# Performance work log

Hardware: AMD Instinct MI355X
Metric: run time of the kernel (lower is better)

## Reference

```python
import jax, jax.numpy as jnp
import numpy as np

INV_SQRT2 = 0.7071067811865476  # 1/sqrt(2), haar filter coefficient
LEVEL = 2
EFF = 3          # effective modes per axis: (16 // omega=6) + 1
OUT_C = 64
SUBBANDS = ("aad", "ada", "add", "daa", "dad", "dda", "ddd")


def dwt1(x, axis):
    # Haar analysis along `axis` (even length, periodic => no padding needed).
    x = jnp.moveaxis(x, axis, -1)
    e, o = x[..., ::2], x[..., 1::2]
    a = (e + o) * INV_SQRT2
    d = (e - o) * INV_SQRT2
    return jnp.moveaxis(a, -1, axis), jnp.moveaxis(d, -1, axis)


def idwt1(a, d, axis):
    a = jnp.moveaxis(a, axis, -1)
    d = jnp.moveaxis(d, axis, -1)
    e = (a + d) * INV_SQRT2
    o = (a - d) * INV_SQRT2
    x = jnp.stack([e, o], axis=-1).reshape(e.shape[:-1] + (2 * e.shape[-1],))
    return jnp.moveaxis(x, -1, axis)


def dwt3(x):
    # One level of separable 3D DWT over last 3 axes -> dict of 8 subbands.
    ax, dx = dwt1(x, -3)
    out = {}
    for nx, tx in (("a", ax), ("d", dx)):
        ay, dy = dwt1(tx, -2)
        for ny, ty in (("a", ay), ("d", dy)):
            az, dz = dwt1(ty, -1)
            out[nx + ny + "a"] = az
            out[nx + ny + "d"] = dz
    return out


def idwt3(c):
    aa = idwt1(c["aaa"], c["aad"], -1)
    ad = idwt1(c["ada"], c["add"], -1)
    da = idwt1(c["daa"], c["dad"], -1)
    dd = idwt1(c["dda"], c["ddd"], -1)
    a = idwt1(aa, ad, -2)
    d = idwt1(da, dd, -2)
    return idwt1(a, d, -3)


def spectralconv(waves, w4):
    # waves: [B, Ci, X, Y, Z] real; w4: [4, Ci, Co, m, m, m] complex.
    B, Ci, X, Y, Z = waves.shape
    m = EFF
    xw = jnp.fft.rfftn(waves, axes=(-3, -2, -1))
    out = jnp.zeros((B, OUT_C, X, Y, Z // 2 + 1), dtype=xw.dtype)
    mul = lambda blk, w: jnp.einsum("bixyz,ioxyz->boxyz", blk, w)
    out = out.at[:, :, :m, :m, :m].set(mul(xw[:, :, :m, :m, :m], w4[0]))
    out = out.at[:, :, -m:, :m, :m].set(mul(xw[:, :, -m:, :m, :m], w4[1]))
    out = out.at[:, :, :m, -m:, :m].set(mul(xw[:, :, :m, -m:, :m], w4[2]))
    out = out.at[:, :, -m:, -m:, :m].set(mul(xw[:, :, -m:, -m:, :m], w4[3]))
    return jnp.fft.irfftn(out, s=(X, Y, Z), axes=(-3, -2, -1))


def _forward(x, weights):
    # weights: [8, 4, Ci, Co, m, m, m, 2] real -> complex [8, 4, Ci, Co, m, m, m]
    w = jax.lax.complex(weights[..., 0], weights[..., 1])
    # multi-level wavedec3: details[0] = finest, details[-1] = coarsest
    a = x
    details = []
    for _ in range(LEVEL):
        c = dwt3(a)
        a = c.pop("aaa")
        details.append(c)
    # spectral conv on coarsest approx + 7 coarsest detail subbands
    a = spectralconv(a, w[0])
    coarse = details[-1]
    details[-1] = {k: spectralconv(coarse[k], w[i + 1]) for i, k in enumerate(SUBBANDS)}
    # waverec3
    for c in reversed(details):
        full = dict(c)
        full["aaa"] = a
        a = idwt3(full)
    return a


def setup_inputs() -> dict:
    key = jax.random.key(0)
    kx, kw = jax.random.split(key)
    x = jax.random.normal(kx, (4, 64, 64, 64, 64), dtype=jnp.float32)
    scale = 1.0 / (64 * 64)
    weights = scale * jax.random.uniform(kw, (8, 4, 64, 64, 3, 3, 3, 2), dtype=jnp.float32)
    return {"x": x, "weights": weights}


def reference(x, weights):
    return _forward(x, weights)
```

## Files before the change

kernel.cpp:

```cpp
#include <hip/hip_runtime.h>


typedef float f32x4 __attribute__((ext_vector_type(4)));

__constant__ float C16c[16] = {
  1.0f, 0.92387953251128675f, 0.70710678118654752f, 0.38268343236508977f,
  0.0f, -0.38268343236508977f, -0.70710678118654752f, -0.92387953251128675f,
  -1.0f, -0.92387953251128675f, -0.70710678118654752f, -0.38268343236508977f,
  0.0f, 0.38268343236508977f, 0.70710678118654752f, 0.92387953251128675f
};
__constant__ float S16c[16] = {
  0.0f, 0.38268343236508977f, 0.70710678118654752f, 0.92387953251128675f,
  1.0f, 0.92387953251128675f, 0.70710678118654752f, 0.38268343236508977f,
  0.0f, -0.38268343236508977f, -0.70710678118654752f, -0.92387953251128675f,
  -1.0f, -0.92387953251128675f, -0.70710678118654752f, -0.38268343236508977f
};
__constant__ int KYv[6] = {0, 1, 2, 13, 14, 15};

__global__ __launch_bounds__(256) void k1_front(const float* __restrict__ x,
                                                float2* __restrict__ g2) {
  __shared__ float sm[8 * 16 * 17 + 8];
  __shared__ float2 fz[8 * 3 * 17];
  unsigned tid = threadIdx.x;
  unsigned px = blockIdx.x & 15u;
  unsigned bc = blockIdx.x >> 4;
  unsigned c = bc & 63u, b = bc >> 6;
  const f32x4* xp4 = (const f32x4*)(x + ((size_t)bc << 18)) + (size_t)px * 4096u;
  unsigned z4 = tid & 15u;
#pragma unroll
  for (int q = 0; q < 4; q++) {
    float a00 = 0.f, a01 = 0.f, a10 = 0.f, a11 = 0.f;
#pragma unroll
    for (int i = 0; i < 4; i++) {
      f32x4 v = xp4[i * 1024 + q * 256 + tid];
      float h0 = v.x + v.y, h1 = v.z + v.w;
      a00 += h0; a01 += h1;
      if (i < 2) { a10 += h0; a11 += h1; } else { a10 -= h0; a11 -= h1; }
    }
    float p00 = a00 + __shfl_xor(a00, 16);
    float p01 = a01 + __shfl_xor(a01, 16);
    float p10 = a10 + __shfl_xor(a10, 16);
    float p11 = a11 + __shfl_xor(a11, 16);
    float q00 = __shfl_xor(p00, 32), q01 = __shfl_xor(p01, 32);
    float q10 = __shfl_xor(p10, 32), q11 = __shfl_xor(p11, 32);
    bool hi = (tid >> 5) & 1u;
    float ya0 = p00 + q00, yd0 = hi ? (q00 - p00) : (p00 - q00);
    float ya1 = p01 + q01, yd1 = hi ? (q01 - p01) : (p01 - q01);
    float za0 = p10 + q10, zd0 = hi ? (q10 - p10) : (p10 - q10);
    float za1 = p11 + q11, zd1 = hi ? (q11 - p11) : (p11 - q11);
    if (((tid >> 4) & 3u) == 0u) {
      unsigned py = q * 4 + (tid >> 6);
      float* smp = sm + py * 17u + z4;
      smp[0 * 272] = (ya0 + ya1) * 0.125f;
      smp[1 * 272] = (ya0 - ya1) * 0.125f;
      smp[2 * 272] = (yd0 + yd1) * 0.125f;
      smp[3 * 272] = (yd0 - yd1) * 0.125f;
      smp[4 * 272] = (za0 + za1) * 0.125f;
      smp[5 * 272] = (za0 - za1) * 0.125f;
      smp[6 * 272] = (zd0 + zd1) * 0.125f;
      smp[7 * 272] = (zd0 - zd1) * 0.125f;
    }
  }
  __syncthreads();
  if (tid < 128u) {
    unsigned k = tid >> 4, y = tid & 15u;
    const float* row = sm + k * 272u + y * 17u;
#pragma unroll
    for (int kz = 0; kz < 3; kz++) {
      float re = 0.f, im = 0.f;
#pragma unroll
      for (int nz = 0; nz < 16; nz++) {
        float vv = row[nz];
        int t16 = (kz * nz) & 15;
        re += vv * C16c[t16];
        im -= vv * S16c[t16];
      }
      fz[k * 51u + kz * 17u + y] = make_float2(re, im);
    }
  }
  __syncthreads();
  if (tid < 144u) {
    unsigned k = tid / 18u, r = tid - k * 18u;
    unsigned kyi = r / 3u, kz = r - kyi * 3u;
    int ky = KYv[kyi];
    float re = 0.f, im = 0.f;
#pragma unroll
    for (int ny = 0; ny < 16; ny++) {
      float2 vv = fz[k * 51u + kz * 17u + ny];
      int t16 = (ky * ny) & 15;
      float cc = C16c[t16], sn = S16c[t16];
      re += vv.x * cc + vv.y * sn;
      im += vv.y * cc - vv.x * sn;
    }
    g2[(((size_t)b * 144u + tid) * 16u + px) * 64u + c] = make_float2(re, im);
  }
}

__global__ __launch_bounds__(256) void k2_mix(const float* __restrict__ w2,
                                              const float2* __restrict__ g2,
                                              float2* __restrict__ oh2) {
  __shared__ float2 ihl[4][64][27];
  unsigned tid = threadIdx.x;
  unsigned kc = blockIdx.x >> 3;
  unsigned ob = blockIdx.x & 7u;
  unsigned k = kc >> 2, corner = kc & 3u;
  unsigned kxi0 = 3u * (corner & 1u), kyi0 = 3u * (corner >> 1);
  {
    unsigned c = tid & 63u, b = tid >> 6;
    const float2* gb = g2 + ((size_t)b * 144u * 16u) * 64u + c;
#pragma unroll
    for (unsigned kyl = 0; kyl < 3u; kyl++) {
#pragma unroll
      for (unsigned kz = 0; kz < 3u; kz++) {
        unsigned row = k * 18u + (kyl + kyi0) * 3u + kz;
        float2 rg[16];
#pragma unroll
        for (int nx = 0; nx < 16; nx++) rg[nx] = gb[((size_t)row * 16u + nx) * 64u];
#pragma unroll
        for (unsigned kxl = 0; kxl < 3u; kxl++) {
          int kx = KYv[kxl + kxi0];
          float re = 0.f, im = 0.f;
#pragma unroll
          for (int nx = 0; nx < 16; nx++) {
            int t16 = (kx * nx) & 15;
            float cc = C16c[t16], sn = S16c[t16];
            re += rg[nx].x * cc + rg[nx].y * sn;
            im += rg[nx].y * cc - rg[nx].x * sn;
          }
          ihl[b][c][kxl * 9u + kyl * 3u + kz] = make_float2(re, im);
        }
      }
    }
  }
  __syncthreads();
  if (tid >= 216u) return;
  unsigned o = tid / 27u, f = tid - o * 27u;
  const float* wp = w2 + (((size_t)kc * 64u * 64u + (ob * 8u + o)) * 27u + f) * 2u;
  float2 acc[4];
#pragma unroll
  for (int b = 0; b < 4; b++) acc[b] = make_float2(0.f, 0.f);
#pragma unroll 8
  for (unsigned i = 0; i < 64u; i++) {
    float wr = __builtin_nontemporal_load(wp + (size_t)i * 3456u);
    float wi = __builtin_nontemporal_load(wp + (size_t)i * 3456u + 1u);
#pragma unroll
    for (int b = 0; b < 4; b++) {
      float2 a = ihl[b][i][f];
      acc[b].x += a.x * wr - a.y * wi;
      acc[b].y += a.x * wi + a.y * wr;
    }
  }
  unsigned kxl = f / 9u, kyl = (f - kxl * 9u) / 3u, kz = f % 3u;
  unsigned fg = (kxl + kxi0) * 18u + (kyl + kyi0) * 3u + kz;
#pragma unroll
  for (int b = 0; b < 4; b++)
    oh2[((size_t)(b * 64u + ob * 8u + o)) * 864u + k * 108u + fg] = acc[b];
}

__global__ __launch_bounds__(256) void k3_invsynth(const float2* __restrict__ oh2,
                                                   const float* __restrict__ x,
                                                   float* __restrict__ out) {
  __shared__ float2 hh[864];
  __shared__ float2 gx[2][8][18];
  __shared__ float2 uu[2][8][3][16];
  __shared__ float W[2][8][16][16];
  unsigned tid = threadIdx.x;
  unsigned sp = blockIdx.x & 7u;
  unsigned bo = 255u - (blockIdx.x >> 3);
  for (unsigned i = tid; i < 864u; i += 256u)
    hh[i] = oh2[(size_t)bo * 864u + i];
  __syncthreads();
  for (unsigned i = tid; i < 288u; i += 256u) {
    unsigned sl = i / 144u, j = i - sl * 144u;
    unsigned k = j / 18u, r = j - k * 18u;
    unsigned nx = sp * 2u + sl;
    float re = 0.f, im = 0.f;
#pragma unroll
    for (int kxi = 0; kxi < 6; kxi++) {
      float2 v = hh[k * 108u + kxi * 18 + r];
      int t16 = (KYv[kxi] * (int)nx) & 15;
      float cc = C16c[t16], sn = S16c[t16];
      re += v.x * cc - v.y * sn;
      im += v.x * sn + v.y * cc;
    }
    gx[sl][k][r] = make_float2(re, im);
  }
  __syncthreads();
  for (unsigned i = tid; i < 768u; i += 256u) {
    unsigned sl = i / 384u, j = i - sl * 384u;
    unsigned k = j / 48u, rem = j - k * 48u;
    unsigned kz = rem >> 4, ny = rem & 15u;
    float re = 0.f, im = 0.f;
#pragma unroll
    for (int kyi = 0; kyi < 6; kyi++) {
      float2 v = gx[sl][k][kyi * 3 + kz];
      int t16 = (KYv[kyi] * (int)ny) & 15;
      float cc = C16c[t16], sn = S16c[t16];
      re += v.x * cc - v.y * sn;
      im += v.x * sn + v.y * cc;
    }
    uu[sl][k][kz][ny] = make_float2(re, im);
  }
  __syncthreads();
  for (unsigned i = tid; i < 512u; i += 256u) {
    unsigned sl = i >> 8, ny = (i >> 4) & 15u, nz = i & 15u;
    float c1 = C16c[nz], s1 = S16c[nz];
    int t2 = (2 * nz) & 15;
    float c2 = C16c[t2], s2 = S16c[t2];
    float val[8];
#pragma unroll
    for (int k = 0; k < 8; k++) {
      float2 u0 = uu[sl][k][0][ny], u1 = uu[sl][k][1][ny], u2 = uu[sl][k][2][ny];
      val[k] = (u0.x + 2.f * (u1.x * c1 - u1.y * s1) + 2.f * (u2.x * c2 - u2.y * s2)) * (1.f / 4096.f);
    }
#pragma unroll
    for (int st = 1; st < 8; st <<= 1)
#pragma unroll
      for (int i2 = 0; i2 < 8; i2++)
        if (!(i2 & st)) {
          float a = val[i2], bb = val[i2 | st];
          val[i2] = a + bb;
          val[i2 | st] = a - bb;
        }
#pragma unroll
    for (int m = 0; m < 8; m++) W[sl][m][ny][nz] = val[m];
  }
  __syncthreads();
  unsigned w = tid >> 6, l = tid & 63u;
  unsigned z4 = l & 15u, y2 = l >> 4;
  unsigned mmy = ((y2 >> 1) & 1u) << 1;
  const float* xp = x + ((size_t)bo << 18);
  float* op = out + ((size_t)bo << 18);
#pragma unroll
  for (unsigned sl = 0; sl < 2u; ++sl) {
#pragma unroll
    for (unsigned r2 = 0; r2 < 8u; ++r2) {
      unsigned xp2 = r2 & 1u, yg = r2 >> 1;
      unsigned X0 = ((sp * 2u + sl) << 2) + (xp2 << 1);
      unsigned Y = (yg << 4) + (w << 2) + y2;
      size_t off = ((size_t)X0 << 12) + (Y << 6) + (z4 << 2);
      f32x4 v0 = *(const f32x4*)(xp + off);
      f32x4 v1 = *(const f32x4*)(xp + off + 4096u);
      float h0 = v0.x + v0.y + v1.x + v1.y;
      float h1 = v0.z + v0.w + v1.z + v1.w;
      float m0 = (h0 + __shfl_xor(h0, 16)) * 0.125f;
      float m1 = (h1 + __shfl_xor(h1, 16)) * 0.125f;
      unsigned ny = (yg << 2) + w;
      unsigned mm = (xp2 << 2) | mmy;
      float c0 = 0.125f * W[sl][mm][ny][z4] - m0;
      float c1 = 0.125f * W[sl][mm | 1u][ny][z4] - m1;
      v0.x += c0; v0.y += c0; v0.z += c1; v0.w += c1;
      v1.x += c0; v1.y += c0; v1.z += c1; v1.w += c1;
      __builtin_nontemporal_store(v0, (f32x4*)(op + off));
      __builtin_nontemporal_store(v1, (f32x4*)(op + off + 4096u));
    }
  }
}

extern "C" void kernel_launch(void* const* d_in, const int* in_sizes, int n_in,
                              void* d_out, int out_size, void* d_ws, size_t ws_size,
                              hipStream_t stream) {
  const float* x = (const float*)d_in[0];
  const float* w = (const float*)d_in[1];
  float* out = (float*)d_out;

  const size_t G_B = 4ull * 144 * 16 * 64 * 8;
  const size_t OH_B = 256ull * 864 * 8;

  float2 *g2, *oh2;
  char* ws = (char*)d_ws;
  if (ws_size >= G_B + OH_B) {
    g2 = (float2*)ws;
    oh2 = (float2*)(ws + G_B);
  } else {
    oh2 = (float2*)ws;
    g2 = (float2*)((char*)d_out + (size_t)out_size * 4 - G_B);
  }

  k1_front<<<4096, 256, 0, stream>>>(x, g2);
  k2_mix<<<256, 256, 0, stream>>>(w, g2, oh2);
  k3_invsynth<<<2048, 256, 0, stream>>>(oh2, x, out);
}
```

Measured before the change: 154.9 us.

## Spread k1 DFT stages across more threads and alias k3 shared memory

In k1, the z-DFT stage now gives each thread a single (k,y,kz) output instead of three, and the y-DFT stage splits each output's 16-term sum into two halves reduced through a new shared buffer, so more threads take part. k3 overlays hh and W in one shared byte array to cut LDS footprint, aiming for higher occupancy. k3's store loop also pairs the two X slabs per iteration so four loads are in flight before the stores. These changes add an extra barrier in k1 and more live registers in k3.

```diff
diff --git a/kernel.cpp b/kernel.cpp
--- a/kernel.cpp
+++ b/kernel.cpp
@@ -19,8 +19,9 @@
 
 __global__ __launch_bounds__(256) void k1_front(const float* __restrict__ x,
                                                 float2* __restrict__ g2) {
-  __shared__ float sm[8 * 16 * 17 + 8];
-  __shared__ float2 fz[8 * 3 * 17];
+  __shared__ float sm[8 * 272 + 8];
+  __shared__ float2 fz[8 * 51];
+  __shared__ float2 ps[288];
   unsigned tid = threadIdx.x;
   unsigned px = blockIdx.x & 15u;
   unsigned bc = blockIdx.x >> 4;
@@ -62,37 +63,44 @@
     }
   }
   __syncthreads();
-  if (tid < 128u) {
-    unsigned k = tid >> 4, y = tid & 15u;
+  for (unsigned it = tid; it < 384u; it += 256u) {
+    unsigned k = it / 48u, rem = it - k * 48u;
+    unsigned y = rem / 3u, kz = rem - y * 3u;
     const float* row = sm + k * 272u + y * 17u;
-#pragma unroll
-    for (int kz = 0; kz < 3; kz++) {
-      float re = 0.f, im = 0.f;
-#pragma unroll
-      for (int nz = 0; nz < 16; nz++) {
-        float vv = row[nz];
-        int t16 = (kz * nz) & 15;
-        re += vv * C16c[t16];
-        im -= vv * S16c[t16];
-      }
-      fz[k * 51u + kz * 17u + y] = make_float2(re, im);
-    }
-  }
-  __syncthreads();
-  if (tid < 144u) {
-    unsigned k = tid / 18u, r = tid - k * 18u;
+    float re = 0.f, im = 0.f;
+#pragma unroll
+    for (int nz = 0; nz < 16; nz++) {
+      float vv = row[nz];
+      int t16 = (kz * nz) & 15;
+      re += vv * C16c[t16];
+      im -= vv * S16c[t16];
+    }
+    fz[k * 51u + kz * 17u + y] = make_float2(re, im);
+  }
+  __syncthreads();
+  for (unsigned it = tid; it < 288u; it += 256u) {
+    unsigned r144 = it >> 1, h = it & 1u;
+    unsigned k = r144 / 18u, r = r144 - k * 18u;
     unsigned kyi = r / 3u, kz = r - kyi * 3u;
     int ky = KYv[kyi];
     float re = 0.f, im = 0.f;
-#pragma unroll
-    for (int ny = 0; ny < 16; ny++) {
+    unsigned ny0 = h * 8u;
+#pragma unroll
+    for (unsigned j = 0; j < 8u; j++) {
+      unsigned ny = ny0 + j;
       float2 vv = fz[k * 51u + kz * 17u + ny];
-      int t16 = (ky * ny) & 15;
+      int t16 = ((unsigned)ky * ny) & 15;
       float cc = C16c[t16], sn = S16c[t16];
       re += vv.x * cc + vv.y * sn;
       im += vv.y * cc - vv.x * sn;
     }
-    g2[(((size_t)b * 144u + tid) * 16u + px) * 64u + c] = make_float2(re, im);
+    ps[it] = make_float2(re, im);
+  }
+  __syncthreads();
+  if (tid < 144u) {
+    float2 a = ps[2u * tid], bb = ps[2u * tid + 1u];
+    g2[(((size_t)b * 144u + tid) * 16u + px) * 64u + c] =
+        make_float2(a.x + bb.x, a.y + bb.y);
   }
 }
 
@@ -160,10 +168,11 @@
 __global__ __launch_bounds__(256) void k3_invsynth(const float2* __restrict__ oh2,
                                                    const float* __restrict__ x,
                                                    float* __restrict__ out) {
-  __shared__ float2 hh[864];
-  __shared__ float2 gx[2][8][18];
-  __shared__ float2 uu[2][8][3][16];
-  __shared__ float W[2][8][16][16];
+  __shared__ __align__(16) unsigned char smem3[24832];
+  float2* hh = (float2*)smem3;
+  float* W = (float*)smem3;
+  float2* uu = (float2*)(smem3 + 16384);
+  float2* gx = (float2*)(smem3 + 22528);
   unsigned tid = threadIdx.x;
   unsigned sp = blockIdx.x & 7u;
   unsigned bo = 255u - (blockIdx.x >> 3);
@@ -183,7 +192,7 @@
       re += v.x * cc - v.y * sn;
       im += v.x * sn + v.y * cc;
     }
-    gx[sl][k][r] = make_float2(re, im);
+    gx[(sl * 8u + k) * 18u + r] = make_float2(re, im);
   }
   __syncthreads();
   for (unsigned i = tid; i < 768u; i += 256u) {
@@ -193,13 +202,13 @@
     float re = 0.f, im = 0.f;
 #pragma unroll
     for (int kyi = 0; kyi < 6; kyi++) {
-      float2 v = gx[sl][k][kyi * 3 + kz];
+      float2 v = gx[(sl * 8u + k) * 18u + kyi * 3 + kz];
       int t16 = (KYv[kyi] * (int)ny) & 15;
       float cc = C16c[t16], sn = S16c[t16];
       re += v.x * cc - v.y * sn;
       im += v.x * sn + v.y * cc;
     }
-    uu[sl][k][kz][ny] = make_float2(re, im);
+    uu[((sl * 8u + k) * 3u + kz) * 16u + ny] = make_float2(re, im);
   }
   __syncthreads();
   for (unsigned i = tid; i < 512u; i += 256u) {
@@ -210,7 +219,9 @@
     float val[8];
 #pragma unroll
     for (int k = 0; k < 8; k++) {
-      float2 u0 = uu[sl][k][0][ny], u1 = uu[sl][k][1][ny], u2 = uu[sl][k][2][ny];
+      float2 u0 = uu[((sl * 8u + k) * 3u + 0) * 16u + ny];
+      float2 u1 = uu[((sl * 8u + k) * 3u + 1) * 16u + ny];
+      float2 u2 = uu[((sl * 8u + k) * 3u + 2) * 16u + ny];
       val[k] = (u0.x + 2.f * (u1.x * c1 - u1.y * s1) + 2.f * (u2.x * c2 - u2.y * s2)) * (1.f / 4096.f);
     }
 #pragma unroll
@@ -223,7 +234,7 @@
           val[i2 | st] = a - bb;
         }
 #pragma unroll
-    for (int m = 0; m < 8; m++) W[sl][m][ny][nz] = val[m];
+    for (int m = 0; m < 8; m++) W[((sl * 8u + m) * 16u + ny) * 16u + nz] = val[m];
   }
   __syncthreads();
   unsigned w = tid >> 6, l = tid & 63u;
@@ -234,25 +245,43 @@
 #pragma unroll
   for (unsigned sl = 0; sl < 2u; ++sl) {
 #pragma unroll
-    for (unsigned r2 = 0; r2 < 8u; ++r2) {
-      unsigned xp2 = r2 & 1u, yg = r2 >> 1;
-      unsigned X0 = ((sp * 2u + sl) << 2) + (xp2 << 1);
+    for (unsigned yg = 0; yg < 4u; ++yg) {
       unsigned Y = (yg << 4) + (w << 2) + y2;
-      size_t off = ((size_t)X0 << 12) + (Y << 6) + (z4 << 2);
-      f32x4 v0 = *(const f32x4*)(xp + off);
-      f32x4 v1 = *(const f32x4*)(xp + off + 4096u);
-      float h0 = v0.x + v0.y + v1.x + v1.y;
-      float h1 = v0.z + v0.w + v1.z + v1.w;
-      float m0 = (h0 + __shfl_xor(h0, 16)) * 0.125f;
-      float m1 = (h1 + __shfl_xor(h1, 16)) * 0.125f;
       unsigned ny = (yg << 2) + w;
-      unsigned mm = (xp2 << 2) | mmy;
-      float c0 = 0.125f * W[sl][mm][ny][z4] - m0;
-      float c1 = 0.125f * W[sl][mm | 1u][ny][z4] - m1;
-      v0.x += c0; v0.y += c0; v0.z += c1; v0.w += c1;
-      v1.x += c0; v1.y += c0; v1.z += c1; v1.w += c1;
-      __builtin_nontemporal_store(v0, (f32x4*)(op + off));
-      __builtin_nontemporal_store(v1, (f32x4*)(op + off + 4096u));
+      unsigned Xa = ((sp * 2u + sl) << 2);
+      unsigned Xb = Xa + 2u;
+      size_t offa = ((size_t)Xa << 12) + (Y << 6) + (z4 << 2);
+      size_t offb = ((size_t)Xb << 12) + (Y << 6) + (z4 << 2);
+      f32x4 v0a = *(const f32x4*)(xp + offa);
+      f32x4 v1a = *(const f32x4*)(xp + offa + 4096u);
+      f32x4 v0b = *(const f32x4*)(xp + offb);
+      f32x4 v1b = *(const f32x4*)(xp + offb + 4096u);
+      {
+        float h0 = v0a.x + v0a.y + v1a.x + v1a.y;
+        float h1 = v0a.z + v0a.w + v1a.z + v1a.w;
+        float m0 = (h0 + __shfl_xor(h0, 16)) * 0.125f;
+        float m1 = (h1 + __shfl_xor(h1, 16)) * 0.125f;
+        unsigned mm = mmy;
+        float c0 = 0.125f * W[((sl * 8u + mm) * 16u + ny) * 16u + z4] - m0;
+        float c1 = 0.125f * W[((sl * 8u + (mm | 1u)) * 16u + ny) * 16u + z4] - m1;
+        v0a.x += c0; v0a.y += c0; v0a.z += c1; v0a.w += c1;
+        v1a.x += c0; v1a.y += c0; v1a.z += c1; v1a.w += c1;
+      }
+      {
+        float h0 = v0b.x + v0b.y + v1b.x + v1b.y;
+        float h1 = v0b.z + v0b.w + v1b.z + v1b.w;
+        float m0 = (h0 + __shfl_xor(h0, 16)) * 0.125f;
+        float m1 = (h1 + __shfl_xor(h1, 16)) * 0.125f;
+        unsigned mm = 4u | mmy;
+        float c0 = 0.125f * W[((sl * 8u + mm) * 16u + ny) * 16u + z4] - m0;
+        float c1 = 0.125f * W[((sl * 8u + (mm | 1u)) * 16u + ny) * 16u + z4] - m1;
+        v0b.x += c0; v0b.y += c0; v0b.z += c1; v0b.w += c1;
+        v1b.x += c0; v1b.y += c0; v1b.z += c1; v1b.w += c1;
+      }
+      __builtin_nontemporal_store(v0a, (f32x4*)(op + offa));
+      __builtin_nontemporal_store(v1a, (f32x4*)(op + offa + 4096u));
+      __builtin_nontemporal_store(v0b, (f32x4*)(op + offb));
+      __builtin_nontemporal_store(v1b, (f32x4*)(op + offb + 4096u));
     }
   }
 }
```

After: 165.8 us. +7.0%, slower.

## Run the three-kernel pipeline in two batch halves for cache reuse

Applied to the files above, without the earlier changes.

Splits the batch into two halves and launches front, mix and inverse-synthesis kernels once per half instead of once for the whole batch. The likely aim is that the half-sized slice of x read by the front kernel stays resident in the large last-level cache when the synthesis kernel reads x again, cutting DRAM traffic. In exchange the mix kernel streams the weights twice, uses only half its threads for the DFT stage, and there are three extra launches with smaller grids.

```diff
diff --git a/kernel.cpp b/kernel.cpp
--- a/kernel.cpp
+++ b/kernel.cpp
@@ -18,12 +18,13 @@
 __constant__ int KYv[6] = {0, 1, 2, 13, 14, 15};
 
 __global__ __launch_bounds__(256) void k1_front(const float* __restrict__ x,
-                                                float2* __restrict__ g2) {
-  __shared__ float sm[8 * 16 * 17 + 8];
-  __shared__ float2 fz[8 * 3 * 17];
+                                                float2* __restrict__ g2,
+                                                int half) {
+  __shared__ float sm[8 * 272 + 8];
+  __shared__ float2 fz[8 * 51];
   unsigned tid = threadIdx.x;
   unsigned px = blockIdx.x & 15u;
-  unsigned bc = blockIdx.x >> 4;
+  unsigned bc = (unsigned)half * 128u + (blockIdx.x >> 4);
   unsigned c = bc & 63u, b = bc >> 6;
   const f32x4* xp4 = (const f32x4*)(x + ((size_t)bc << 18)) + (size_t)px * 4096u;
   unsigned z4 = tid & 15u;
@@ -98,15 +99,17 @@
 
 __global__ __launch_bounds__(256) void k2_mix(const float* __restrict__ w2,
                                               const float2* __restrict__ g2,
-                                              float2* __restrict__ oh2) {
-  __shared__ float2 ihl[4][64][27];
+                                              float2* __restrict__ oh2,
+                                              int half) {
+  __shared__ float2 ihl[2][64][27];
   unsigned tid = threadIdx.x;
   unsigned kc = blockIdx.x >> 3;
   unsigned ob = blockIdx.x & 7u;
   unsigned k = kc >> 2, corner = kc & 3u;
   unsigned kxi0 = 3u * (corner & 1u), kyi0 = 3u * (corner >> 1);
-  {
-    unsigned c = tid & 63u, b = tid >> 6;
+  if (tid < 128u) {
+    unsigned c = tid & 63u, b2 = tid >> 6;
+    unsigned b = (unsigned)half * 2u + b2;
     const float2* gb = g2 + ((size_t)b * 144u * 16u) * 64u + c;
 #pragma unroll
     for (unsigned kyl = 0; kyl < 3u; kyl++) {
@@ -127,7 +130,7 @@
             re += rg[nx].x * cc + rg[nx].y * sn;
             im += rg[nx].y * cc - rg[nx].x * sn;
           }
-          ihl[b][c][kxl * 9u + kyl * 3u + kz] = make_float2(re, im);
+          ihl[b2][c][kxl * 9u + kyl * 3u + kz] = make_float2(re, im);
         }
       }
     }
@@ -136,37 +139,40 @@
   if (tid >= 216u) return;
   unsigned o = tid / 27u, f = tid - o * 27u;
   const float* wp = w2 + (((size_t)kc * 64u * 64u + (ob * 8u + o)) * 27u + f) * 2u;
-  float2 acc[4];
-#pragma unroll
-  for (int b = 0; b < 4; b++) acc[b] = make_float2(0.f, 0.f);
+  float2 acc[2];
+#pragma unroll
+  for (int b2 = 0; b2 < 2; b2++) acc[b2] = make_float2(0.f, 0.f);
 #pragma unroll 8
   for (unsigned i = 0; i < 64u; i++) {
     float wr = __builtin_nontemporal_load(wp + (size_t)i * 3456u);
     float wi = __builtin_nontemporal_load(wp + (size_t)i * 3456u + 1u);
 #pragma unroll
-    for (int b = 0; b < 4; b++) {
-      float2 a = ihl[b][i][f];
-      acc[b].x += a.x * wr - a.y * wi;
-      acc[b].y += a.x * wi + a.y * wr;
+    for (int b2 = 0; b2 < 2; b2++) {
+      float2 a = ihl[b2][i][f];
+      acc[b2].x += a.x * wr - a.y * wi;
+      acc[b2].y += a.x * wi + a.y * wr;
     }
   }
   unsigned kxl = f / 9u, kyl = (f - kxl * 9u) / 3u, kz = f % 3u;
   unsigned fg = (kxl + kxi0) * 18u + (kyl + kyi0) * 3u + kz;
 #pragma unroll
-  for (int b = 0; b < 4; b++)
-    oh2[((size_t)(b * 64u + ob * 8u + o)) * 864u + k * 108u + fg] = acc[b];
+  for (int b2 = 0; b2 < 2; b2++) {
+    unsigned b = (unsigned)half * 2u + (unsigned)b2;
+    oh2[((size_t)(b * 64u + ob * 8u + o)) * 864u + k * 108u + fg] = acc[b2];
+  }
 }
 
 __global__ __launch_bounds__(256) void k3_invsynth(const float2* __restrict__ oh2,
                                                    const float* __restrict__ x,
-                                                   float* __restrict__ out) {
+                                                   float* __restrict__ out,
+                                                   int half) {
   __shared__ float2 hh[864];
   __shared__ float2 gx[2][8][18];
   __shared__ float2 uu[2][8][3][16];
   __shared__ float W[2][8][16][16];
   unsigned tid = threadIdx.x;
   unsigned sp = blockIdx.x & 7u;
-  unsigned bo = 255u - (blockIdx.x >> 3);
+  unsigned bo = (unsigned)half * 128u + (127u - (blockIdx.x >> 3));
   for (unsigned i = tid; i < 864u; i += 256u)
     hh[i] = oh2[(size_t)bo * 864u + i];
   __syncthreads();
@@ -277,7 +283,9 @@
     g2 = (float2*)((char*)d_out + (size_t)out_size * 4 - G_B);
   }
 
-  k1_front<<<4096, 256, 0, stream>>>(x, g2);
-  k2_mix<<<256, 256, 0, stream>>>(w, g2, oh2);
-  k3_invsynth<<<2048, 256, 0, stream>>>(oh2, x, out);
-}
+  for (int half = 0; half < 2; ++half) {
+    k1_front<<<2048, 256, 0, stream>>>(x, g2, half);
+    k2_mix<<<256, 256, 0, stream>>>(w, g2, oh2, half);
+    k3_invsynth<<<1024, 256, 0, stream>>>(oh2, x, out, half);
+  }
+}
```

Result: slower. 185.3 us (+19.6%).
